# Optimization experiments

Hardware: AMD Instinct MI355X
Metric: run time of the kernel (lower is better)

Reference implementation:

```python
import jax, jax.numpy as jnp
import numpy as np
from jax import lax

B, DIM, RES = 1024, 384, 7
HEADS, KEY_DIM, ATTN_RATIO = 8, 32, 4
N = RES * RES            # 49
KH = KEY_DIM * HEADS     # 256
D = ATTN_RATIO * KEY_DIM # 128
DH = D * HEADS           # 1024
SCALE = KEY_DIM ** -0.5


def _rel_pos_idx():
    ii, jj = np.meshgrid(np.arange(RES), np.arange(RES), indexing='ij')
    pos = np.stack([ii.ravel(), jj.ravel()])          # [2, N]
    rel = np.abs(pos[:, :, None] - pos[:, None, :])   # [2, N, N]
    return jnp.asarray(rel[0] * RES + rel[1])         # [N, N] int

REL_IDX = _rel_pos_idx()


def conv1x1_bn(x, w, b, s, o):
    # 1x1 conv (pointwise GEMM) + eval-mode BatchNorm folded to scale/shift
    y = jnp.einsum('oc,bchw->bohw', w, x) + b[:, None, None]
    return y * s[:, None, None] + o[:, None, None]


def setup_inputs() -> dict:
    key = jax.random.key(0)
    ks = jax.random.split(key, 32)
    f = lambda i, shape, scale=0.02: jax.random.normal(ks[i], shape, jnp.float32) * scale
    u = lambda i, shape: jax.random.uniform(ks[i], shape, jnp.float32, 0.5, 1.5)
    inp = {
        'x': jax.random.normal(ks[0], (B, DIM, RES, RES), jnp.float32),
        'q_w': f(1, (KH, DIM)), 'q_b': f(2, (KH,)), 'q_s': u(3, (KH,)), 'q_o': f(4, (KH,)),
        'k_w': f(5, (KH, DIM)), 'k_b': f(6, (KH,)), 'k_s': u(7, (KH,)), 'k_o': f(8, (KH,)),
        'v_w': f(9, (DH, DIM)), 'v_b': f(10, (DH,)), 'v_s': u(11, (DH,)), 'v_o': f(12, (DH,)),
        'vl_w': f(13, (DH, 1, 3, 3)), 'vl_b': f(14, (DH,)), 'vl_s': u(15, (DH,)), 'vl_o': f(16, (DH,)),
        'th1_w': f(17, (HEADS, HEADS), 0.1), 'th1_b': f(18, (HEADS,)),
        'th2_w': f(19, (HEADS, HEADS), 0.1), 'th2_b': f(20, (HEADS,)),
        'p_w': f(21, (DIM, DH)), 'p_b': f(22, (DIM,)), 'p_s': u(23, (DIM,)), 'p_o': f(24, (DIM,)),
        'ab': f(25, (HEADS, N), 0.1),
    }
    return inp


def reference(x, q_w, q_b, q_s, q_o, k_w, k_b, k_s, k_o, v_w, v_b, v_s, v_o,
              vl_w, vl_b, vl_s, vl_o, th1_w, th1_b, th2_w, th2_b,
              p_w, p_b, p_s, p_o, ab):
    b = x.shape[0]
    q = conv1x1_bn(x, q_w, q_b, q_s, q_o).reshape(b, HEADS, KEY_DIM, N)
    q = q.transpose(0, 1, 3, 2)                         # [B,H,N,kd]
    k = conv1x1_bn(x, k_w, k_b, k_s, k_o).reshape(b, HEADS, KEY_DIM, N)  # [B,H,kd,N]
    v4 = conv1x1_bn(x, v_w, v_b, v_s, v_o)              # [B,DH,7,7]
    # local depthwise 3x3 branch + BN
    vl = lax.conv_general_dilated(v4, vl_w, (1, 1), 'SAME',
                                  feature_group_count=DH,
                                  dimension_numbers=('NCHW', 'OIHW', 'NCHW'))
    vl = (vl + vl_b[:, None, None]) * vl_s[:, None, None] + vl_o[:, None, None]
    v = v4.reshape(b, HEADS, D, N).transpose(0, 1, 3, 2)  # [B,H,N,d]

    bias = ab[:, REL_IDX]                                # [H,N,N]
    attn = jnp.einsum('bhnd,bhdm->bhnm', q, k) * SCALE + bias[None]
    # talking head 1 (1x1 conv over head dim)
    attn = jnp.einsum('ij,bjnm->binm', th1_w, attn) + th1_b[None, :, None, None]
    attn = jax.nn.softmax(attn, axis=-1)
    # talking head 2
    attn = jnp.einsum('ij,bjnm->binm', th2_w, attn) + th2_b[None, :, None, None]

    out = jnp.einsum('bhnm,bhmd->bhnd', attn, v)         # [B,H,N,d]
    out = out.transpose(0, 1, 3, 2).reshape(b, DH, RES, RES) + vl
    out = jax.nn.gelu(out, approximate=False)            # nn.GELU default = exact
    out = conv1x1_bn(out, p_w, p_b, p_s, p_o)            # [B,DIM,7,7]
    return out
```

## Files before the change

### kernel.cpp

```cpp
#include <hip/hip_runtime.h>
#include <math.h>

typedef unsigned short u16;
typedef unsigned int u32;
typedef short short8 __attribute__((ext_vector_type(8)));
typedef float f32x4 __attribute__((ext_vector_type(4)));
typedef unsigned int u32x2 __attribute__((ext_vector_type(2)));

#define SCALE_QK 0.17677669529663687f
#define PSLAB 23296

__device__ __forceinline__ float b2f(u16 v) { return __uint_as_float(((u32)v) << 16); }
__device__ __forceinline__ u16 f2b(float f) {
  u32 u = __float_as_uint(f);
  return (u16)((u + 0x7fffu + ((u >> 16) & 1u)) >> 16);
}

__device__ __forceinline__ float gelu_f(float z) {
  float y = z * 0.70710678118654752f;
  float a = fabsf(y);
  float t = __builtin_amdgcn_rcpf(fmaf(0.3275911f, a, 1.0f));
  float e = __expf(-y * y);
  float p = fmaf(1.061405429f, t, -1.453152027f);
  p = fmaf(p, t, 1.421413741f);
  p = fmaf(p, t, -0.284496736f);
  p = fmaf(p, t, 0.254829592f);
  p = p * t * e;
  float phi = (y >= 0.f) ? fmaf(-0.5f, p, 1.0f) : 0.5f * p;
  return z * phi;
}

__global__ __launch_bounds__(256) void k_pre(
    const float* __restrict__ th1w, const float* __restrict__ th1b, const float* __restrict__ ab,
    const float* __restrict__ qb, const float* __restrict__ qs, const float* __restrict__ qo,
    const float* __restrict__ kb, const float* __restrict__ ks, const float* __restrict__ ko,
    const float* __restrict__ vb, const float* __restrict__ vs, const float* __restrict__ vo,
    const float* __restrict__ pb, const float* __restrict__ ps, const float* __restrict__ po,
    const float* __restrict__ qw, const float* __restrict__ kw,
    const float* __restrict__ vw, const float* __restrict__ pw,
    float* __restrict__ bias2, float* __restrict__ alpha, float* __restrict__ beta,
    float* __restrict__ alphap, float* __restrict__ betap,
    u16* __restrict__ Wqk, u16* __restrict__ Wv, u16* __restrict__ Wp)
{
  int gid = blockIdx.x * 256 + threadIdx.x;
  if (gid < 19208) {
    int i = gid / 2401, rem = gid % 2401, n = rem / 49, m = rem % 49;
    int ry = abs(n / 7 - m / 7), rx = abs(n % 7 - m % 7);
    int idx = ry * 7 + rx;
    float acc = th1b[i];
    #pragma unroll
    for (int j = 0; j < 8; j++) acc += th1w[i * 8 + j] * ab[j * 49 + idx];
    bias2[gid] = acc;
  } else if (gid < 20744) {
    int c = gid - 19208;
    const float *s, *bb, *oo; int idx;
    if (c < 256)      { s = qs; bb = qb; oo = qo; idx = c; }
    else if (c < 512) { s = ks; bb = kb; oo = ko; idx = c - 256; }
    else              { s = vs; bb = vb; oo = vo; idx = c - 512; }
    float sv = s[idx];
    alpha[c] = sv;
    beta[c] = sv * bb[idx] + oo[idx];
  } else if (gid < 21128) {
    int c = gid - 20744;
    float sv = ps[c];
    alphap[c] = sv;
    betap[c] = sv * pb[c] + po[c];
  } else {
    int g = gid - 21128;
    if (g < 98304)       Wqk[g] = f2b(qw[g]);
    else if (g < 196608) Wqk[g] = f2b(kw[g - 98304]);
    else if (g < 589824) Wv[g - 196608] = f2b(vw[g - 196608]);
    else if (g < 983040) Wp[g - 589824] = f2b(pw[g - 589824]);
  }
}

__global__ __launch_bounds__(512, 4) void k_qk(
    const float* __restrict__ x, const u16* __restrict__ Wqk,
    const float* __restrict__ alpha, const float* __restrict__ beta,
    u16* __restrict__ Pbuf, u16* __restrict__ XTg)
{
  __shared__ __align__(16) u16 lds[37376];
  u16* XT = lds;
  u16* Tq = lds + 26112;
  u16* Tk = lds + 31744;
  int t = threadIdx.x, wv = t >> 6, l = t & 63, quad = l >> 4, l16 = l & 15;
  int b = blockIdx.x;
  const float* xb = x + (size_t)b * 18816;

  for (int e = t; e < 18816; e += 512) {
    int k = e / 49, n = e - k * 49;
    XT[n * 408 + k] = f2b(xb[e]);
  }
  for (int e = t; e < 3060; e += 512) {
    int r = e / 204, kk = e - r * 204;
    ((u32*)(XT + (49 + r) * 408))[kk] = 0;
  }
  __syncthreads();

  if (XTg) {
    u32* dst = (u32*)(XTg + (size_t)b * 24576);
    const u32* src32 = (const u32*)XT;
    for (int e = t; e < 12288; e += 512) {
      int row = e / 192, cc = e - row * 192;
      dst[e] = src32[row * 204 + cc];
    }
  }

  u16* Pg = Pbuf + (size_t)b * PSLAB;
  int isK = wv >= 4, wl = wv & 3;
  for (int hp = 0; hp < 4; hp++) {
    int cbase = (isK ? 256 : 0) + hp * 64 + wl * 16;
    f32x4 acc[4] = {};
    const u16* Wr = Wqk + (size_t)(cbase + l16) * 384;
    short8 afr[12];
    #pragma unroll
    for (int ks = 0; ks < 12; ks++) afr[ks] = *(const short8*)(Wr + ks * 32 + quad * 8);
    #pragma unroll
    for (int ks = 0; ks < 12; ks++) {
      #pragma unroll
      for (int nt = 0; nt < 4; nt++) {
        short8 bf = *(const short8*)(&XT[(nt * 16 + l16) * 408 + ks * 32 + quad * 8]);
        acc[nt] = __builtin_amdgcn_mfma_f32_16x16x32_bf16(afr[ks], bf, acc[nt], 0, 0, 0);
      }
    }
    u16* Tdst = isK ? Tk : Tq;
    #pragma unroll
    for (int reg = 0; reg < 4; reg++) {
      int c = cbase + quad * 4 + reg;
      float al = alpha[c], be = beta[c];
      int cl = wl * 16 + quad * 4 + reg;
      #pragma unroll
      for (int nt = 0; nt < 4; nt++)
        Tdst[(nt * 16 + l16) * 88 + cl] = f2b(acc[nt][reg] * al + be);
    }
    __syncthreads();
    #pragma unroll
    for (int ui = 0; ui < 4; ui++) {
      int u = wv * 4 + ui;
      int hl = u >> 4, tn = (u >> 2) & 3, tm = u & 3;
      short8 a  = *(const short8*)(&Tq[(tn * 16 + l16) * 88 + hl * 32 + quad * 8]);
      short8 bb = *(const short8*)(&Tk[(tm * 16 + l16) * 88 + hl * 32 + quad * 8]);
      f32x4 c = {};
      c = __builtin_amdgcn_mfma_f32_16x16x32_bf16(a, bb, c, 0, 0, 0);
      int h = hp * 2 + hl;
      #pragma unroll
      for (int r = 0; r < 4; r++) {
        int n = tn * 16 + quad * 4 + r, m = tm * 16 + l16;
        if (n < 52 && m < 56)
          Pg[(h * 52 + n) * 56 + m] = (n < 49 && m < 49) ? f2b(c[r] * SCALE_QK) : (u16)0;
      }
    }
    __syncthreads();
  }
}

__global__ __launch_bounds__(256, 4) void k_mix(
    u16* __restrict__ Pbuf, const float* __restrict__ bias2,
    const float* __restrict__ th1w, const float* __restrict__ th1b,
    const float* __restrict__ th2w, const float* __restrict__ th2b)
{
  __shared__ u16 SB[23296];
  __shared__ float TH[144];
  int t = threadIdx.x, b = blockIdx.x;
  u32* Pg32 = (u32*)(Pbuf + (size_t)b * PSLAB);
  for (int e = t; e < 11648; e += 256) ((u32*)SB)[e] = Pg32[e];
  if (t < 64)       TH[t] = th1w[t];
  else if (t < 72)  TH[t] = th1b[t - 64];
  else if (t < 136) TH[t] = th2w[t - 72];
  else if (t < 144) TH[t] = th2b[t - 136];
  __syncthreads();
  for (int e = t; e < 2401; e += 256) {
    int n = e / 49, m = e - n * 49;
    float s[8], uo[8];
    #pragma unroll
    for (int j = 0; j < 8; j++) s[j] = b2f(SB[(j * 52 + n) * 56 + m]);
    #pragma unroll
    for (int i = 0; i < 8; i++) {
      float a2 = bias2[(i * 49 + n) * 49 + m];
      #pragma unroll
      for (int j = 0; j < 8; j++) a2 += TH[i * 8 + j] * s[j];
      uo[i] = a2;
    }
    #pragma unroll
    for (int i = 0; i < 8; i++) SB[(i * 52 + n) * 56 + m] = f2b(uo[i]);
  }
  __syncthreads();
  for (int r0 = t; r0 < 392; r0 += 256) {
    int i = r0 / 49, n = r0 - i * 49;
    u16* row = &SB[(i * 52 + n) * 56];
    float v[49]; float mx = -1e30f;
    #pragma unroll
    for (int m = 0; m < 49; m++) { v[m] = b2f(row[m]); mx = fmaxf(mx, v[m]); }
    float sum = 0.f;
    #pragma unroll
    for (int m = 0; m < 49; m++) { v[m] = __expf(v[m] - mx); sum += v[m]; }
    float inv = 1.f / sum;
    #pragma unroll
    for (int m = 0; m < 49; m++) row[m] = f2b(v[m] * inv);
  }
  __syncthreads();
  for (int e = t; e < 2401; e += 256) {
    int n = e / 49, m = e - n * 49;
    float s[8], uo[8];
    #pragma unroll
    for (int j = 0; j < 8; j++) s[j] = b2f(SB[(j * 52 + n) * 56 + m]);
    #pragma unroll
    for (int i = 0; i < 8; i++) {
      float a2 = TH[136 + i];
      #pragma unroll
      for (int j = 0; j < 8; j++) a2 += TH[72 + i * 8 + j] * s[j];
      uo[i] = a2;
    }
    #pragma unroll
    for (int i = 0; i < 8; i++) SB[(i * 52 + n) * 56 + m] = f2b(uo[i]);
  }
  __syncthreads();
  for (int e = t; e < 11648; e += 256) Pg32[e] = ((u32*)SB)[e];
}

__global__ __launch_bounds__(512, 4) void k_av_x(
    const u16* __restrict__ XTg, const u16* __restrict__ Wv,
    const float* __restrict__ alpha, const float* __restrict__ beta,
    const float* __restrict__ vlw, const float* __restrict__ vlb,
    const float* __restrict__ vls, const float* __restrict__ vlo,
    const u16* __restrict__ Pbuf, u16* __restrict__ Zs)
{
  __shared__ __align__(16) u16 lds[38968];
  u16* XT = lds;
  u16* VT = lds + 26112;
  u16* Ph = lds + 35328;
  int t = threadIdx.x, wv = t >> 6, l = t & 63, quad = l >> 4, l16 = l & 15;
  int b = blockIdx.x;

  {
    const short8* src8 = (const short8*)(XTg + (size_t)b * 24576);
    for (int e = t; e < 3072; e += 512) {
      int row = e / 48, cc = e - row * 48;
      *(short8*)(XT + row * 408 + cc * 8) = src8[e];
    }
  }
  for (int e = t; e < 4608; e += 512) ((u32*)VT)[e] = 0;
  __syncthreads();

  u16* Zb = Zs + (size_t)b * 50176;
  const u16* Pgb = Pbuf + (size_t)b * PSLAB;
  for (int h = 0; h < 8; h++) {
    {
      const u32* src = (const u32*)(Pgb + h * 2912);
      for (int e = t; e < 1456; e += 512) ((u32*)Ph)[e] = src[e];
    }
    const u16* Wr = Wv + (size_t)(h * 128 + wv * 16 + l16) * 384;
    short8 afr[12];
    #pragma unroll
    for (int ks = 0; ks < 12; ks++) afr[ks] = *(const short8*)(Wr + ks * 32 + quad * 8);
    int d = wv * 16 + l16, c = h * 128 + d;
    float w9[9];
    #pragma unroll
    for (int j = 0; j < 9; j++) w9[j] = vlw[c * 9 + j];
    float sv = vls[c];
    float cb = sv * vlb[c] + vlo[c];

    f32x4 va[4] = {};
    #pragma unroll
    for (int ks = 0; ks < 12; ks++) {
      #pragma unroll
      for (int nt = 0; nt < 4; nt++) {
        short8 bf = *(const short8*)(&XT[(nt * 16 + l16) * 408 + ks * 32 + quad * 8]);
        va[nt] = __builtin_amdgcn_mfma_f32_16x16x32_bf16(afr[ks], bf, va[nt], 0, 0, 0);
      }
    }
    #pragma unroll
    for (int reg = 0; reg < 4; reg++) {
      int dl = wv * 16 + quad * 4 + reg;
      int cc = h * 128 + dl;
      float al = alpha[512 + cc], be = beta[512 + cc];
      #pragma unroll
      for (int nt = 0; nt < 4; nt++) {
        int m = nt * 16 + l16;
        if (m < 49) VT[dl * 72 + 8 + m] = f2b(va[nt][reg] * al + be);
      }
    }
    __syncthreads();
    f32x4 oa[4] = {};
    #pragma unroll
    for (int ks2 = 0; ks2 < 2; ks2++) {
      int mb = ks2 * 32 + quad * 8;
      short8 bf = *(const short8*)(&VT[(wv * 16 + l16) * 72 + 8 + mb]);
      #pragma unroll
      for (int tn = 0; tn < 4; tn++) {
        short8 af = *(const short8*)(&Ph[(tn * 16 + l16) * 56 + mb]);
        oa[tn] = __builtin_amdgcn_mfma_f32_16x16x32_bf16(af, bf, oa[tn], 0, 0, 0);
      }
    }
    const u16* vtr = &VT[d * 72];
    #pragma unroll
    for (int tn = 0; tn < 4; tn++) {
      int n0 = tn * 16 + quad * 4;
      const u16* vr = vtr + n0;
      float q[20];
      #pragma unroll
      for (int jj = 0; jj < 5; jj++) {
        u32x2 U = *(const u32x2*)(vr + jj * 4);
        q[jj * 4 + 0] = __uint_as_float(U.x << 16);
        q[jj * 4 + 1] = __uint_as_float(U.x & 0xffff0000u);
        q[jj * 4 + 2] = __uint_as_float(U.y << 16);
        q[jj * 4 + 3] = __uint_as_float(U.y & 0xffff0000u);
      }
      #pragma unroll
      for (int r = 0; r < 4; r++) {
        int n = n0 + r;
        int yi = (n * 37) >> 8;
        int xi = n - yi * 7;
        bool xl = xi > 0, xr = xi < 6;
        float w0m = xl ? w9[0] : 0.f, w3m = xl ? w9[3] : 0.f, w6m = xl ? w9[6] : 0.f;
        float w2m = xr ? w9[2] : 0.f, w5m = xr ? w9[5] : 0.f, w8m = xr ? w9[8] : 0.f;
        float conv = q[r]      * w0m + q[r + 1]  * w9[1] + q[r + 2]  * w2m
                   + q[r + 7]  * w3m + q[r + 8]  * w9[4] + q[r + 9]  * w5m
                   + q[r + 14] * w6m + q[r + 15] * w9[7] + q[r + 16] * w8m;
        float z = oa[tn][r] + conv * sv + cb;
        float g = gelu_f(z);
        if (n < 49) Zb[(size_t)n * 1024 + c] = f2b(g);
      }
    }
    __syncthreads();
  }
}

__global__ __launch_bounds__(512, 4) void k_av_fb(
    const float* __restrict__ x, const u16* __restrict__ Wv,
    const float* __restrict__ alpha, const float* __restrict__ beta,
    const float* __restrict__ vlw, const float* __restrict__ vlb,
    const float* __restrict__ vls, const float* __restrict__ vlo,
    const u16* __restrict__ Pbuf, u16* __restrict__ Zs)
{
  __shared__ __align__(16) u16 lds[38968];
  u16* XT = lds;
  u16* VT = lds + 26112;
  u16* Ph = lds + 35328;
  int t = threadIdx.x, wv = t >> 6, l = t & 63, quad = l >> 4, l16 = l & 15;
  int b = blockIdx.x;
  const float* xb = x + (size_t)b * 18816;

  for (int e = t; e < 18816; e += 512) {
    int k = e / 49, n = e - k * 49;
    XT[n * 408 + k] = f2b(xb[e]);
  }
  for (int e = t; e < 3060; e += 512) {
    int r = e / 204, kk = e - r * 204;
    ((u32*)(XT + (49 + r) * 408))[kk] = 0;
  }
  for (int e = t; e < 4608; e += 512) ((u32*)VT)[e] = 0;
  __syncthreads();

  u16* Zb = Zs + (size_t)b * 50176;
  const u16* Pgb = Pbuf + (size_t)b * PSLAB;
  for (int h = 0; h < 8; h++) {
    {
      const u32* src = (const u32*)(Pgb + h * 2912);
      for (int e = t; e < 1456; e += 512) ((u32*)Ph)[e] = src[e];
    }
    const u16* Wr = Wv + (size_t)(h * 128 + wv * 16 + l16) * 384;
    short8 afr[12];
    #pragma unroll
    for (int ks = 0; ks < 12; ks++) afr[ks] = *(const short8*)(Wr + ks * 32 + quad * 8);
    int d = wv * 16 + l16, c = h * 128 + d;
    float w9[9];
    #pragma unroll
    for (int j = 0; j < 9; j++) w9[j] = vlw[c * 9 + j];
    float sv = vls[c];
    float cb = sv * vlb[c] + vlo[c];

    f32x4 va[4] = {};
    #pragma unroll
    for (int ks = 0; ks < 12; ks++) {
      #pragma unroll
      for (int nt = 0; nt < 4; nt++) {
        short8 bf = *(const short8*)(&XT[(nt * 16 + l16) * 408 + ks * 32 + quad * 8]);
        va[nt] = __builtin_amdgcn_mfma_f32_16x16x32_bf16(afr[ks], bf, va[nt], 0, 0, 0);
      }
    }
    #pragma unroll
    for (int reg = 0; reg < 4; reg++) {
      int dl = wv * 16 + quad * 4 + reg;
      int cc = h * 128 + dl;
      float al = alpha[512 + cc], be = beta[512 + cc];
      #pragma unroll
      for (int nt = 0; nt < 4; nt++) {
        int m = nt * 16 + l16;
        if (m < 49) VT[dl * 72 + 8 + m] = f2b(va[nt][reg] * al + be);
      }
    }
    __syncthreads();
    f32x4 oa[4] = {};
    #pragma unroll
    for (int ks2 = 0; ks2 < 2; ks2++) {
      int mb = ks2 * 32 + quad * 8;
      short8 bf = *(const short8*)(&VT[(wv * 16 + l16) * 72 + 8 + mb]);
      #pragma unroll
      for (int tn = 0; tn < 4; tn++) {
        short8 af = *(const short8*)(&Ph[(tn * 16 + l16) * 56 + mb]);
        oa[tn] = __builtin_amdgcn_mfma_f32_16x16x32_bf16(af, bf, oa[tn], 0, 0, 0);
      }
    }
    const u16* vtr = &VT[d * 72];
    #pragma unroll
    for (int tn = 0; tn < 4; tn++) {
      int n0 = tn * 16 + quad * 4;
      const u16* vr = vtr + n0;
      float q[20];
      #pragma unroll
      for (int jj = 0; jj < 5; jj++) {
        u32x2 U = *(const u32x2*)(vr + jj * 4);
        q[jj * 4 + 0] = __uint_as_float(U.x << 16);
        q[jj * 4 + 1] = __uint_as_float(U.x & 0xffff0000u);
        q[jj * 4 + 2] = __uint_as_float(U.y << 16);
        q[jj * 4 + 3] = __uint_as_float(U.y & 0xffff0000u);
      }
      #pragma unroll
      for (int r = 0; r < 4; r++) {
        int n = n0 + r;
        int yi = (n * 37) >> 8;
        int xi = n - yi * 7;
        bool xl = xi > 0, xr = xi < 6;
        float w0m = xl ? w9[0] : 0.f, w3m = xl ? w9[3] : 0.f, w6m = xl ? w9[6] : 0.f;
        float w2m = xr ? w9[2] : 0.f, w5m = xr ? w9[5] : 0.f, w8m = xr ? w9[8] : 0.f;
        float conv = q[r]      * w0m + q[r + 1]  * w9[1] + q[r + 2]  * w2m
                   + q[r + 7]  * w3m + q[r + 8]  * w9[4] + q[r + 9]  * w5m
                   + q[r + 14] * w6m + q[r + 15] * w9[7] + q[r + 16] * w8m;
        float z = oa[tn][r] + conv * sv + cb;
        float g = gelu_f(z);
        if (n < 49) Zb[(size_t)n * 1024 + c] = f2b(g);
      }
    }
    __syncthreads();
  }
}

__global__ __launch_bounds__(512, 4) void k_proj(
    const u16* __restrict__ Wp, const u16* __restrict__ Zt,
    const float* __restrict__ alphap, const float* __restrict__ betap,
    float* __restrict__ out)
{
  __shared__ __align__(16) u16 Bs[128 * 152];
  int t = threadIdx.x, wv = t >> 6, l = t & 63, quad = l >> 4, l16 = l & 15;
  int g = blockIdx.x;
  int vb = (g & 7) * 192 + (g >> 3);
  int mb = vb % 3;
  size_t b0 = (size_t)(vb / 3) * 2;
  f32x4 acc[8] = {};
  const u16* Wr = Wp + (size_t)(mb * 128 + wv * 16 + l16) * 1024;
  for (int k0 = 0; k0 < 1024; k0 += 128) {
    #pragma unroll
    for (int i = 0; i < 4; i++) {
      int ch = t + i * 512;
      int np = ch >> 4, ck = ch & 15;
      int pb = np >> 6, n = np & 63;
      short8 v = {};
      if (n < 49)
        v = *(const short8*)(Zt + (b0 + pb) * 50176 + (size_t)n * 1024 + k0 + ck * 8);
      *(short8*)(&Bs[np * 152 + ck * 8]) = v;
    }
    __syncthreads();
    #pragma unroll
    for (int ksi = 0; ksi < 4; ksi++) {
      short8 af = *(const short8*)(Wr + k0 + ksi * 32 + quad * 8);
      #pragma unroll
      for (int nt = 0; nt < 8; nt++) {
        short8 bf = *(const short8*)(&Bs[(nt * 16 + l16) * 152 + ksi * 32 + quad * 8]);
        acc[nt] = __builtin_amdgcn_mfma_f32_16x16x32_bf16(af, bf, acc[nt], 0, 0, 0);
      }
    }
    __syncthreads();
  }
  #pragma unroll
  for (int reg = 0; reg < 4; reg++) {
    int c = mb * 128 + wv * 16 + quad * 4 + reg;
    float al = alphap[c], be = betap[c];
    #pragma unroll
    for (int nt = 0; nt < 8; nt++) {
      int np = nt * 16 + l16, pb = np >> 6, n = np & 63;
      if (n < 49) out[(b0 + pb) * 18816 + (size_t)c * 49 + n] = acc[nt][reg] * al + be;
    }
  }
}

extern "C" void kernel_launch(void* const* d_in, const int* in_sizes, int n_in,
                              void* d_out, int out_size, void* d_ws, size_t ws_size,
                              hipStream_t stream) {
  const float* x    = (const float*)d_in[0];
  const float* qw   = (const float*)d_in[1];
  const float* qb   = (const float*)d_in[2];
  const float* qs   = (const float*)d_in[3];
  const float* qo   = (const float*)d_in[4];
  const float* kw   = (const float*)d_in[5];
  const float* kb   = (const float*)d_in[6];
  const float* ks   = (const float*)d_in[7];
  const float* ko   = (const float*)d_in[8];
  const float* vw   = (const float*)d_in[9];
  const float* vb   = (const float*)d_in[10];
  const float* vs   = (const float*)d_in[11];
  const float* vo   = (const float*)d_in[12];
  const float* vlw  = (const float*)d_in[13];
  const float* vlb  = (const float*)d_in[14];
  const float* vls  = (const float*)d_in[15];
  const float* vlo  = (const float*)d_in[16];
  const float* th1w = (const float*)d_in[17];
  const float* th1b = (const float*)d_in[18];
  const float* th2w = (const float*)d_in[19];
  const float* th2b = (const float*)d_in[20];
  const float* pw   = (const float*)d_in[21];
  const float* pb   = (const float*)d_in[22];
  const float* ps   = (const float*)d_in[23];
  const float* po   = (const float*)d_in[24];
  const float* ab   = (const float*)d_in[25];
  float* out = (float*)d_out;
  char* ws = (char*)d_ws;

  u16* Pbuf = (u16*)d_out;

  float* bias2  = (float*)(ws + 0);
  float* alpha  = (float*)(ws + 77056);
  float* beta   = (float*)(ws + 83200);
  float* alphap = (float*)(ws + 89344);
  float* betap  = (float*)(ws + 90880);
  u16*   Wqk16  = (u16*)(ws + 92416);
  u16*   Wv16   = (u16*)(ws + 485632);
  u16*   Wp16   = (u16*)(ws + 1272064);
  u16*   Zs     = (u16*)(ws + 2058496);
  bool big = ws_size >= 155150592ull;
  u16*   XTg    = big ? (u16*)(ws + 104818944) : (u16*)nullptr;

  k_pre<<<3923, 256, 0, stream>>>(th1w, th1b, ab, qb, qs, qo, kb, ks, ko,
                                  vb, vs, vo, pb, ps, po, qw, kw, vw, pw,
                                  bias2, alpha, beta, alphap, betap,
                                  Wqk16, Wv16, Wp16);
  k_qk<<<1024, 512, 0, stream>>>(x, Wqk16, alpha, beta, Pbuf, XTg);
  k_mix<<<1024, 256, 0, stream>>>(Pbuf, bias2, th1w, th1b, th2w, th2b);
  if (big)
    k_av_x<<<1024, 512, 0, stream>>>(XTg, Wv16, alpha, beta, vlw, vlb, vls, vlo, Pbuf, Zs);
  else
    k_av_fb<<<1024, 512, 0, stream>>>(x, Wv16, alpha, beta, vlw, vlb, vls, vlo, Pbuf, Zs);
  k_proj<<<1536, 512, 0, stream>>>(Wp16, Zs, alphap, betap, out);
}
```

Measured before the change: 553.0 us.

## Split fused V-projection/attention kernel into separate V GEMM and PV kernels

When the workspace is large enough, the fused k_av_x kernel is replaced by two kernels. k_vg computes the V projection with BN into a global bf16 buffer. k_pv then loads V per head, does the attention-times-V MFMA, the depthwise 3x3 conv, BN and GELU. Each kernel uses less LDS and allows higher occupancy, at the cost of an extra round trip of about 117MB through global memory. The new path only runs when the workspace is at least about 272MB.

```diff
diff --git a/kernel.cpp b/kernel.cpp
--- a/kernel.cpp
+++ b/kernel.cpp
@@ -216,6 +216,141 @@
   }
   __syncthreads();
   for (int e = t; e < 11648; e += 256) Pg32[e] = ((u32*)SB)[e];
+}
+
+__global__ __launch_bounds__(512, 6) void k_vg(
+    const u16* __restrict__ XTg, const u16* __restrict__ Wv,
+    const float* __restrict__ alpha, const float* __restrict__ beta,
+    u16* __restrict__ Vg)
+{
+  __shared__ __align__(16) u16 XT[26112];
+  int t = threadIdx.x, wv = t >> 6, l = t & 63, quad = l >> 4, l16 = l & 15;
+  int b = blockIdx.x;
+
+  {
+    const short8* src8 = (const short8*)(XTg + (size_t)b * 24576);
+    for (int e = t; e < 3072; e += 512) {
+      int row = e / 48, cc = e - row * 48;
+      *(short8*)(XT + row * 408 + cc * 8) = src8[e];
+    }
+  }
+  __syncthreads();
+
+  u16* Vb = Vg + (size_t)b * 57344;
+  for (int h = 0; h < 8; h++) {
+    const u16* Wr = Wv + (size_t)(h * 128 + wv * 16 + l16) * 384;
+    short8 afr[12];
+    #pragma unroll
+    for (int ks = 0; ks < 12; ks++) afr[ks] = *(const short8*)(Wr + ks * 32 + quad * 8);
+    f32x4 va[4] = {};
+    #pragma unroll
+    for (int ks = 0; ks < 12; ks++) {
+      #pragma unroll
+      for (int nt = 0; nt < 4; nt++) {
+        short8 bf = *(const short8*)(&XT[(nt * 16 + l16) * 408 + ks * 32 + quad * 8]);
+        va[nt] = __builtin_amdgcn_mfma_f32_16x16x32_bf16(afr[ks], bf, va[nt], 0, 0, 0);
+      }
+    }
+    #pragma unroll
+    for (int reg = 0; reg < 4; reg++) {
+      int c = h * 128 + wv * 16 + quad * 4 + reg;
+      float al = alpha[512 + c], be = beta[512 + c];
+      #pragma unroll
+      for (int nt = 0; nt < 4; nt++) {
+        int m = nt * 16 + l16;
+        if (m < 49)      Vb[(size_t)c * 56 + m] = f2b(va[nt][reg] * al + be);
+        else if (m < 56) Vb[(size_t)c * 56 + m] = 0;
+      }
+    }
+  }
+}
+
+__global__ __launch_bounds__(512, 8) void k_pv(
+    const u16* __restrict__ Vg,
+    const float* __restrict__ vlw, const float* __restrict__ vlb,
+    const float* __restrict__ vls, const float* __restrict__ vlo,
+    const u16* __restrict__ Pbuf, u16* __restrict__ Zs)
+{
+  __shared__ __align__(16) u16 lds[12856];
+  u16* VT = lds;
+  u16* Ph = lds + 9216;
+  int t = threadIdx.x, wv = t >> 6, l = t & 63, quad = l >> 4, l16 = l & 15;
+  int b = blockIdx.x;
+  int d = wv * 16 + l16;
+
+  for (int e = t; e < 1024; e += 512) {
+    int row = e >> 3, k = e & 7;
+    int col = k < 4 ? k * 2 : 64 + (k - 4) * 2;
+    *(u32*)(&VT[row * 72 + col]) = 0;
+  }
+
+  u16* Zb = Zs + (size_t)b * 50176;
+  const u16* Pgb = Pbuf + (size_t)b * PSLAB;
+  const u16* Vb = Vg + (size_t)b * 57344;
+  for (int h = 0; h < 8; h++) {
+    {
+      const short8* src = (const short8*)(Vb + (size_t)h * 128 * 56);
+      for (int e = t; e < 896; e += 512) {
+        int row = e / 7, cc = e - row * 7;
+        *(short8*)(&VT[row * 72 + 8 + cc * 8]) = src[e];
+      }
+    }
+    {
+      const u32* src = (const u32*)(Pgb + h * 2912);
+      for (int e = t; e < 1456; e += 512) ((u32*)Ph)[e] = src[e];
+    }
+    __syncthreads();
+
+    int c = h * 128 + d;
+    float w9[9];
+    #pragma unroll
+    for (int j = 0; j < 9; j++) w9[j] = vlw[c * 9 + j];
+    float sv = vls[c];
+    float cb = sv * vlb[c] + vlo[c];
+
+    f32x4 oa[4] = {};
+    #pragma unroll
+    for (int ks2 = 0; ks2 < 2; ks2++) {
+      int mb = ks2 * 32 + quad * 8;
+      short8 bf = *(const short8*)(&VT[(wv * 16 + l16) * 72 + 8 + mb]);
+      #pragma unroll
+      for (int tn = 0; tn < 4; tn++) {
+        short8 af = *(const short8*)(&Ph[(tn * 16 + l16) * 56 + mb]);
+        oa[tn] = __builtin_amdgcn_mfma_f32_16x16x32_bf16(af, bf, oa[tn], 0, 0, 0);
+      }
+    }
+    const u16* vtr = &VT[d * 72];
+    #pragma unroll
+    for (int tn = 0; tn < 4; tn++) {
+      int n0 = tn * 16 + quad * 4;
+      const u16* vr = vtr + n0;
+      float q[20];
+      #pragma unroll
+      for (int jj = 0; jj < 5; jj++) {
+        u32x2 U = *(const u32x2*)(vr + jj * 4);
+        q[jj * 4 + 0] = __uint_as_float(U.x << 16);
+        q[jj * 4 + 1] = __uint_as_float(U.x & 0xffff0000u);
+        q[jj * 4 + 2] = __uint_as_float(U.y << 16);
+        q[jj * 4 + 3] = __uint_as_float(U.y & 0xffff0000u);
+      }
+      #pragma unroll
+      for (int r = 0; r < 4; r++) {
+        int n = n0 + r;
+        int yi = (n * 37) >> 8;
+        int xi = n - yi * 7;
+        bool xl = xi > 0, xr = xi < 6;
+        float w0m = xl ? w9[0] : 0.f, w3m = xl ? w9[3] : 0.f, w6m = xl ? w9[6] : 0.f;
+        float w2m = xr ? w9[2] : 0.f, w5m = xr ? w9[5] : 0.f, w8m = xr ? w9[8] : 0.f;
+        float conv = q[r]      * w0m + q[r + 1]  * w9[1] + q[r + 2]  * w2m
+                   + q[r + 7]  * w3m + q[r + 8]  * w9[4] + q[r + 9]  * w5m
+                   + q[r + 14] * w6m + q[r + 15] * w9[7] + q[r + 16] * w8m;
+        float z = oa[tn][r] + conv * sv + cb;
+        float g = gelu_f(z);
+        if (n < 49) Zb[(size_t)n * 1024 + c] = f2b(g);
+      }
+    }
+    __syncthreads();
+  }
 }
 
 __global__ __launch_bounds__(512, 4) void k_av_x(
@@ -527,8 +662,10 @@
   u16*   Wv16   = (u16*)(ws + 485632);
   u16*   Wp16   = (u16*)(ws + 1272064);
   u16*   Zs     = (u16*)(ws + 2058496);
-  bool big = ws_size >= 155150592ull;
-  u16*   XTg    = big ? (u16*)(ws + 104818944) : (u16*)nullptr;
+  bool big  = ws_size >= 155150592ull;
+  bool huge = ws_size >= 272591104ull;
+  u16*   XTg    = big  ? (u16*)(ws + 104818944) : (u16*)nullptr;
+  u16*   Vg     = (u16*)(ws + 155150592);
 
   k_pre<<<3923, 256, 0, stream>>>(th1w, th1b, ab, qb, qs, qo, kb, ks, ko,
                                   vb, vs, vo, pb, ps, po, qw, kw, vw, pw,
@@ -536,9 +673,13 @@
                                   Wqk16, Wv16, Wp16);
   k_qk<<<1024, 512, 0, stream>>>(x, Wqk16, alpha, beta, Pbuf, XTg);
   k_mix<<<1024, 256, 0, stream>>>(Pbuf, bias2, th1w, th1b, th2w, th2b);
-  if (big)
+  if (huge) {
+    k_vg<<<1024, 512, 0, stream>>>(XTg, Wv16, alpha, beta, Vg);
+    k_pv<<<1024, 512, 0, stream>>>(Vg, vlw, vlb, vls, vlo, Pbuf, Zs);
+  } else if (big) {
     k_av_x<<<1024, 512, 0, stream>>>(XTg, Wv16, alpha, beta, vlw, vlb, vls, vlo, Pbuf, Zs);
-  else
+  } else {
     k_av_fb<<<1024, 512, 0, stream>>>(x, Wv16, alpha, beta, vlw, vlb, vls, vlo, Pbuf, Zs);
+  }
   k_proj<<<1536, 512, 0, stream>>>(Wp16, Zs, alphap, betap, out);
 }
```

After: 1.350 ms. 144% more time.

## Double-buffer per-head attention probabilities and drop a block barrier in k_av_x

Applied to the files above, without the earlier changes.

Per-head attention probabilities are now prefetched into registers for the next head and written into an alternate LDS buffer, so the global load overlaps the V projection MFMAs. The mid-loop __syncthreads is replaced by a compiler memory fence, which relies on each wave reading only the VT rows it wrote. The XT row stride changes from 408 to 392 elements, and only the VT padding columns are zeroed instead of the whole buffer. The risks are LDS bank conflicts from the new stride and races on the probability buffers if the remaining barriers no longer order them.

```diff
diff --git a/kernel.cpp b/kernel.cpp
--- a/kernel.cpp
+++ b/kernel.cpp
@@ -225,10 +225,11 @@
     const float* __restrict__ vls, const float* __restrict__ vlo,
     const u16* __restrict__ Pbuf, u16* __restrict__ Zs)
 {
-  __shared__ __align__(16) u16 lds[38968];
-  u16* XT = lds;
-  u16* VT = lds + 26112;
-  u16* Ph = lds + 35328;
+  __shared__ __align__(16) u16 lds[40800];
+  u16* XT  = lds;
+  u16* VT  = lds + 25088;
+  u16* Ph0 = lds + 34304;
+  u16* Ph1 = lds + 37216;
   int t = threadIdx.x, wv = t >> 6, l = t & 63, quad = l >> 4, l16 = l & 15;
   int b = blockIdx.x;
 
@@ -236,24 +237,38 @@
     const short8* src8 = (const short8*)(XTg + (size_t)b * 24576);
     for (int e = t; e < 3072; e += 512) {
       int row = e / 48, cc = e - row * 48;
-      *(short8*)(XT + row * 408 + cc * 8) = src8[e];
-    }
-  }
-  for (int e = t; e < 4608; e += 512) ((u32*)VT)[e] = 0;
+      *(short8*)(XT + row * 392 + cc * 8) = src8[e];
+    }
+  }
+  {
+    int row = wv * 16 + (l >> 2), k2 = (l & 3) * 2;
+    *(u32*)(&VT[row * 72 + k2]) = 0;
+    *(u32*)(&VT[row * 72 + 56 + k2]) = 0;
+    *(u32*)(&VT[row * 72 + 64 + k2]) = 0;
+  }
+  const u16* Pgb = Pbuf + (size_t)b * PSLAB;
+  {
+    const u32* src = (const u32*)Pgb;
+    for (int e = t; e < 1456; e += 512) ((u32*)Ph0)[e] = src[e];
+  }
   __syncthreads();
 
   u16* Zb = Zs + (size_t)b * 50176;
-  const u16* Pgb = Pbuf + (size_t)b * PSLAB;
+  int d = wv * 16 + l16;
   for (int h = 0; h < 8; h++) {
-    {
-      const u32* src = (const u32*)(Pgb + h * 2912);
-      for (int e = t; e < 1456; e += 512) ((u32*)Ph)[e] = src[e];
-    }
-    const u16* Wr = Wv + (size_t)(h * 128 + wv * 16 + l16) * 384;
+    u16* PhR = (h & 1) ? Ph1 : Ph0;
+    u16* PhW = (h & 1) ? Ph0 : Ph1;
+    u32 pr0 = 0, pr1 = 0, pr2 = 0;
+    if (h < 7) {
+      const u32* src = (const u32*)(Pgb + (h + 1) * 2912);
+      pr0 = src[t]; pr1 = src[t + 512];
+      if (t < 432) pr2 = src[t + 1024];
+    }
+    int c = h * 128 + d;
+    const u16* Wr = Wv + (size_t)c * 384;
     short8 afr[12];
     #pragma unroll
     for (int ks = 0; ks < 12; ks++) afr[ks] = *(const short8*)(Wr + ks * 32 + quad * 8);
-    int d = wv * 16 + l16, c = h * 128 + d;
     float w9[9];
     #pragma unroll
     for (int j = 0; j < 9; j++) w9[j] = vlw[c * 9 + j];
@@ -265,7 +280,7 @@
     for (int ks = 0; ks < 12; ks++) {
       #pragma unroll
       for (int nt = 0; nt < 4; nt++) {
-        short8 bf = *(const short8*)(&XT[(nt * 16 + l16) * 408 + ks * 32 + quad * 8]);
+        short8 bf = *(const short8*)(&XT[(nt * 16 + l16) * 392 + ks * 32 + quad * 8]);
         va[nt] = __builtin_amdgcn_mfma_f32_16x16x32_bf16(afr[ks], bf, va[nt], 0, 0, 0);
       }
     }
@@ -280,7 +295,12 @@
         if (m < 49) VT[dl * 72 + 8 + m] = f2b(va[nt][reg] * al + be);
       }
     }
-    __syncthreads();
+    if (h < 7) {
+      u32* dst = (u32*)PhW;
+      dst[t] = pr0; dst[t + 512] = pr1;
+      if (t < 432) dst[t + 1024] = pr2;
+    }
+    asm volatile("" ::: "memory");
     f32x4 oa[4] = {};
     #pragma unroll
     for (int ks2 = 0; ks2 < 2; ks2++) {
@@ -288,7 +308,7 @@
       short8 bf = *(const short8*)(&VT[(wv * 16 + l16) * 72 + 8 + mb]);
       #pragma unroll
       for (int tn = 0; tn < 4; tn++) {
-        short8 af = *(const short8*)(&Ph[(tn * 16 + l16) * 56 + mb]);
+        short8 af = *(const short8*)(&PhR[(tn * 16 + l16) * 56 + mb]);
         oa[tn] = __builtin_amdgcn_mfma_f32_16x16x32_bf16(af, bf, oa[tn], 0, 0, 0);
       }
     }
```

Result: faster. 540.6 us (-2.2%).
